# Kernel tuning notes

Measured on AMD Instinct MI355X. Metric: run time of the kernel, lower is better.

The kernel has to match this reference:

```python
import jax, jax.numpy as jnp
import numpy as np

B, ZD, E, L, NL = 64, 512, 512, 8192, 1000


def irm(x, Ws, bs):
    # IRMLinear(d, n_layers=2): stack of residual linear blocks x <- x + Linear(x)
    for W, b in zip(Ws, bs):
        x = x + x @ W.T + b
    return x


def setup_inputs() -> dict:
    key = jax.random.key(0)
    ks = jax.random.split(key, 10)
    s = lambda k, sh: (jax.random.normal(k, sh, jnp.float32) * 0.02)
    return dict(
        z=jax.random.normal(ks[0], (B, ZD), jnp.float32),
        y=jax.random.randint(ks[1], (B,), 0, NL),
        W_yemb=s(ks[2], (E, NL)), b_yemb=jnp.zeros((E,), jnp.float32),
        Wy1=s(ks[3], (E, E)), by1=jnp.zeros((E,), jnp.float32),
        Wy2=s(ks[4], (E, E)), by2=jnp.zeros((E,), jnp.float32),
        Wz1=s(ks[5], (ZD, ZD)), bz1=jnp.zeros((ZD,), jnp.float32),
        Wz2=s(ks[6], (ZD, ZD)), bz2=jnp.zeros((ZD,), jnp.float32),
        W_zlat=s(ks[7], (L, ZD)),          # Linear(z_dim, lat_size, bias=False)
        w_proj=s(ks[8], (E,)),             # Linear(embed_size, 1, bias=False)
    )


def reference(z, y, W_yemb, b_yemb, Wy1, by1, Wy2, by2, Wz1, bz1, Wz2, bz2, W_zlat, w_proj):
    # y: int64 class ids -> one-hot via identity embedding_mat
    yembed = jax.nn.one_hot(y, NL, dtype=jnp.float32)            # [B, NL]
    ye = yembed @ W_yemb.T + b_yemb                               # [B, E]
    ye = irm(ye, [Wy1, Wy2], [by1, by2])                          # [B, E]
    zz = irm(z, [Wz1, Wz2], [bz1, bz2])                           # [B, ZD]
    zl = zz @ W_zlat.T                                            # [B, L]
    # bmm(z[:,:,1], ye[:,1,:]) then lat_proj over embed collapses to a
    # per-batch scalar: lat[b,i] = zl[b,i] * (ye[b] . w_proj)  (same math,
    # avoids the [B, L, E] intermediate)
    s_scal = ye @ w_proj                                          # [B]
    return zl * s_scal[:, None]                                   # [B, L]
```

## Files before the change

### kernel.cpp

```cpp
#include <hip/hip_runtime.h>


#define BB 64
#define DD 512
#define LL 8192
#define NLBL 1000

typedef __attribute__((ext_vector_type(8))) short short8;
typedef __attribute__((ext_vector_type(4))) float f32x4;

__device__ __forceinline__ unsigned short f2bf(float f) {
  unsigned u = __float_as_uint(f);
  return (unsigned short)((u + 0x7fffu + ((u >> 16) & 1u)) >> 16);
}

__device__ __forceinline__ void matvec_block(int eblk, const float* __restrict__ W,
                                             const float* __restrict__ vin,
                                             float* __restrict__ vout) {
  __shared__ float vl[DD];
  __shared__ float red[256];
  int tid = threadIdx.x;
  vl[tid] = vin[tid];
  vl[tid + 256] = vin[tid + 256];
  __syncthreads();
  int el = tid & 31, jg = tid >> 5;
  int e = eblk * 32 + el;
  float acc = 0.f;
  for (int j = jg; j < DD; j += 8)
    acc += W[j * DD + e] * vl[j];
  red[tid] = acc;
  __syncthreads();
  if (tid < 32) {
    float s = vl[eblk * 32 + tid];
#pragma unroll
    for (int g = 0; g < 8; ++g) s += red[g * 32 + tid];
    vout[eblk * 32 + tid] = s;
  }
}

template <int GATHER, int BF16OUT, int JW, int HASBIAS>
__device__ __forceinline__ void gemm_fullk(
    int blk, const float* __restrict__ Ain,
    const float* __restrict__ Wemb, const float* __restrict__ bemb,
    const int* __restrict__ y,
    const float* __restrict__ W, const float* __restrict__ bias,
    float* __restrict__ outf, unsigned short* __restrict__ outh) {
  __shared__ __align__(16) float As[8][DD];
  int tid = threadIdx.x;
  constexpr int NJT = DD / JW;
  int bt = blk / NJT, jt = blk % NJT;
  int b0 = bt * 8, j0 = jt * JW;
  if (GATHER) {
#pragma unroll
    for (int r = 0; r < 8; ++r) {
      int yb = y[b0 + r];
      As[r][tid]       = Wemb[(size_t)tid * NLBL + yb]         + bemb[tid];
      As[r][tid + 256] = Wemb[(size_t)(tid + 256) * NLBL + yb] + bemb[tid + 256];
    }
  } else {
#pragma unroll
    for (int i = 0; i < 4; ++i) {
      int g = tid + i * 256;
      int row = g >> 7, c4 = (g & 127) << 2;
      *(float4*)&As[row][c4] = *(const float4*)&Ain[(size_t)(b0 + row) * DD + c4];
    }
  }
  __syncthreads();
  int jl = tid & 31, bg = tid >> 5;
  constexpr int NO = JW / 32;
  const float* wr[NO];
#pragma unroll
  for (int o = 0; o < NO; ++o) wr[o] = W + (size_t)(j0 + o * 32 + jl) * DD;
  float a0[NO] = {}, a1[NO] = {}, a2[NO] = {}, a3[NO] = {};
#pragma unroll 4
  for (int k4 = 0; k4 < 128; ++k4) {
    float4 av = *(const float4*)&As[bg][k4 << 2];
#pragma unroll
    for (int o = 0; o < NO; ++o) {
      float4 wv = *(const float4*)&wr[o][k4 << 2];
      a0[o] = fmaf(av.x, wv.x, a0[o]);
      a1[o] = fmaf(av.y, wv.y, a1[o]);
      a2[o] = fmaf(av.z, wv.z, a2[o]);
      a3[o] = fmaf(av.w, wv.w, a3[o]);
    }
  }
#pragma unroll
  for (int o = 0; o < NO; ++o) {
    int j = j0 + o * 32 + jl;
    float v = (a0[o] + a1[o]) + (a2[o] + a3[o]) + As[bg][j];
    if (HASBIAS) v += bias[j];
    if (BF16OUT) outh[(size_t)(b0 + bg) * DD + j] = f2bf(v);
    else         outf[(size_t)(b0 + bg) * DD + j] = v;
  }
}

__device__ __forceinline__ void s_block(int cid, const float* __restrict__ GH,
                                        const float* __restrict__ u1,
                                        const float* __restrict__ by1,
                                        const float* __restrict__ by2,
                                        const float* __restrict__ w_proj,
                                        float* __restrict__ sv) {
  __shared__ float red[256];
  __shared__ float d2s;
  int tid = threadIdx.x;
  float p = by1[tid] * u1[tid] + by2[tid] * w_proj[tid] +
            by1[tid + 256] * u1[tid + 256] + by2[tid + 256] * w_proj[tid + 256];
  red[tid] = p;
  __syncthreads();
  if (tid < 64) {
    float s = red[tid] + red[tid + 64] + red[tid + 128] + red[tid + 192];
#pragma unroll
    for (int d = 32; d; d >>= 1) s += __shfl_down(s, d, 64);
    if (tid == 0) d2s = s;
  }
  __syncthreads();
  int bloc = tid >> 6, lane = tid & 63;
  int b = cid * 4 + bloc;
  int e0 = lane * 8;
  float4 g0 = *(const float4*)&GH[(size_t)b * DD + e0];
  float4 g1 = *(const float4*)&GH[(size_t)b * DD + e0 + 4];
  float4 ua = *(const float4*)&u1[e0];
  float4 ub = *(const float4*)&u1[e0 + 4];
  float sg = g0.x * ua.x + g0.y * ua.y + g0.z * ua.z + g0.w * ua.w +
             g1.x * ub.x + g1.y * ub.y + g1.z * ub.z + g1.w * ub.w;
#pragma unroll
  for (int d = 32; d; d >>= 1) sg += __shfl_down(sg, d, 64);
  if (lane == 0) sv[b] = sg + d2s;
}

__global__ __launch_bounds__(256) void k1(
    const float* __restrict__ z, const float* __restrict__ Wz1,
    const float* __restrict__ bz1, float* __restrict__ X1,
    const float* __restrict__ Wy2, const float* __restrict__ w_proj,
    float* __restrict__ u1, const float* __restrict__ W_yemb,
    const float* __restrict__ b_yemb, const int* __restrict__ y,
    const float* __restrict__ Wy1, float* __restrict__ GH) {
  int blk = blockIdx.x;
  if (blk < 64)
    gemm_fullk<1, 0, 64, 0>(blk, nullptr, W_yemb, b_yemb, y, Wy1, nullptr, GH, nullptr);
  else if (blk < 192)
    gemm_fullk<0, 0, 32, 1>(blk - 64, z, nullptr, nullptr, nullptr, Wz1, bz1, X1, nullptr);
  else
    matvec_block(blk - 192, Wy2, w_proj, u1);
}

__global__ __launch_bounds__(256) void k2(
    const float* __restrict__ X1, const float* __restrict__ Wz2,
    const float* __restrict__ bz2, unsigned short* __restrict__ zzs,
    const float* __restrict__ GH, const float* __restrict__ u1,
    const float* __restrict__ by1, const float* __restrict__ by2,
    const float* __restrict__ w_proj, float* __restrict__ sv) {
  int blk = blockIdx.x;
  if (blk < 128)
    gemm_fullk<0, 1, 32, 1>(blk, X1, nullptr, nullptr, nullptr, Wz2, bz2, nullptr, zzs);
  else
    s_block(blk - 128, GH, u1, by1, by2, w_proj, sv);
}

__global__ __launch_bounds__(256) void kC(const unsigned short* __restrict__ zzs,
                                          const float* __restrict__ W,
                                          const float* __restrict__ sv,
                                          float* __restrict__ out) {
  __shared__ __align__(16) unsigned short Bs[16 * 512];
  __shared__ float ss[64];
  int tid = threadIdx.x;
  int l0 = blockIdx.x * 16;
  if (tid < 64) ss[tid] = sv[tid];
#pragma unroll
  for (int i = 0; i < 4; ++i) {
    int gi = tid + i * 256, row = gi >> 6, c = gi & 63;
    const float* src = &W[(size_t)(l0 + row) * DD + c * 8];
    float4 v0 = *(const float4*)src;
    float4 v1 = *(const float4*)(src + 4);
    short8 h = {(short)f2bf(v0.x), (short)f2bf(v0.y), (short)f2bf(v0.z),
                (short)f2bf(v0.w), (short)f2bf(v1.x), (short)f2bf(v1.y),
                (short)f2bf(v1.z), (short)f2bf(v1.w)};
    *(short8*)&Bs[row * DD + ((c ^ (row & 7)) << 3)] = h;
  }
  __syncthreads();
  int wave = tid >> 6, lane = tid & 63, quad = lane >> 4, l15 = lane & 15;
  const unsigned short* arow = zzs + (wave * 16 + l15) * DD + quad * 8;
  f32x4 acc = {};
  short8 apf[4];
#pragma unroll
  for (int p = 0; p < 4; ++p) apf[p] = *(const short8*)(arow + p * 32);
#pragma unroll
  for (int kc = 0; kc < 4; ++kc) {
    short8 cur[4] = {apf[0], apf[1], apf[2], apf[3]};
    if (kc < 3) {
#pragma unroll
      for (int p = 0; p < 4; ++p)
        apf[p] = *(const short8*)(arow + (kc + 1) * 128 + p * 32);
    }
#pragma unroll
    for (int s = 0; s < 4; ++s) {
      int c = kc * 16 + s * 4 + quad;
      short8 bf = *(const short8*)&Bs[l15 * DD + ((c ^ (l15 & 7)) << 3)];
      acc = __builtin_amdgcn_mfma_f32_16x16x32_bf16(cur[s], bf, acc, 0, 0, 0);
    }
  }
#pragma unroll
  for (int reg = 0; reg < 4; ++reg) {
    int b = wave * 16 + quad * 4 + reg;
    out[(size_t)b * LL + l0 + l15] = acc[reg] * ss[b];
  }
}

extern "C" void kernel_launch(void* const* d_in, const int* in_sizes, int n_in,
                              void* d_out, int out_size, void* d_ws, size_t ws_size,
                              hipStream_t stream) {
  const float* z      = (const float*)d_in[0];
  const int*   y      = (const int*)  d_in[1];
  const float* W_yemb = (const float*)d_in[2];
  const float* b_yemb = (const float*)d_in[3];
  const float* Wy1    = (const float*)d_in[4];
  const float* by1    = (const float*)d_in[5];
  const float* Wy2    = (const float*)d_in[6];
  const float* by2    = (const float*)d_in[7];
  const float* Wz1    = (const float*)d_in[8];
  const float* bz1    = (const float*)d_in[9];
  const float* Wz2    = (const float*)d_in[10];
  const float* bz2    = (const float*)d_in[11];
  const float* W_zlat = (const float*)d_in[12];
  const float* w_proj = (const float*)d_in[13];

  float* ws = (float*)d_ws;
  float* X1 = ws;
  float* GH = ws + 32768;
  float* u1 = ws + 65536;
  float* sv = ws + 66048;
  unsigned short* zzs = (unsigned short*)(ws + 66112);
  float* out = (float*)d_out;

  k1<<<208, 256, 0, stream>>>(z, Wz1, bz1, X1, Wy2, w_proj, u1, W_yemb, b_yemb, y, Wy1, GH);
  k2<<<144, 256, 0, stream>>>(X1, Wz2, bz2, zzs, GH, u1, by1, by2, w_proj, sv);
  kC<<<512, 256, 0, stream>>>(zzs, W_zlat, sv, out);
}
```

Before: 146.9 us.

## Stage weight tiles through double-buffered LDS in small GEMM blocks

```diff
diff --git a/kernel.cpp b/kernel.cpp
--- a/kernel.cpp
+++ b/kernel.cpp
@@ -39,17 +39,20 @@
 }
 
 template <int GATHER, int BF16OUT, int JW, int HASBIAS>
-__device__ __forceinline__ void gemm_fullk(
+__device__ __forceinline__ void gemm_fullk2(
     int blk, const float* __restrict__ Ain,
     const float* __restrict__ Wemb, const float* __restrict__ bemb,
     const int* __restrict__ y,
     const float* __restrict__ W, const float* __restrict__ bias,
     float* __restrict__ outf, unsigned short* __restrict__ outh) {
+  constexpr int NO = JW / 32;
+  constexpr int NJT = DD / JW;
   __shared__ __align__(16) float As[8][DD];
-  int tid = threadIdx.x;
-  constexpr int NJT = DD / JW;
+  __shared__ __align__(16) float Ws[2][JW][68];
+  int tid = threadIdx.x;
   int bt = blk / NJT, jt = blk % NJT;
   int b0 = bt * 8, j0 = jt * JW;
+
   if (GATHER) {
 #pragma unroll
     for (int r = 0; r < 8; ++r) {
@@ -65,24 +68,39 @@
       *(float4*)&As[row][c4] = *(const float4*)&Ain[(size_t)(b0 + row) * DD + c4];
     }
   }
-  __syncthreads();
+#pragma unroll
+  for (int i = 0; i < NO * 2; ++i) {
+    int gi = tid + i * 256;
+    int row = gi >> 4, c4 = (gi & 15) << 2;
+    *(float4*)&Ws[0][row][c4] = *(const float4*)&W[(size_t)(j0 + row) * DD + c4];
+  }
+  __syncthreads();
+
   int jl = tid & 31, bg = tid >> 5;
-  constexpr int NO = JW / 32;
-  const float* wr[NO];
-#pragma unroll
-  for (int o = 0; o < NO; ++o) wr[o] = W + (size_t)(j0 + o * 32 + jl) * DD;
   float a0[NO] = {}, a1[NO] = {}, a2[NO] = {}, a3[NO] = {};
-#pragma unroll 4
-  for (int k4 = 0; k4 < 128; ++k4) {
-    float4 av = *(const float4*)&As[bg][k4 << 2];
-#pragma unroll
-    for (int o = 0; o < NO; ++o) {
-      float4 wv = *(const float4*)&wr[o][k4 << 2];
-      a0[o] = fmaf(av.x, wv.x, a0[o]);
-      a1[o] = fmaf(av.y, wv.y, a1[o]);
-      a2[o] = fmaf(av.z, wv.z, a2[o]);
-      a3[o] = fmaf(av.w, wv.w, a3[o]);
-    }
+  for (int c = 0; c < 8; ++c) {
+    if (c < 7) {
+#pragma unroll
+      for (int i = 0; i < NO * 2; ++i) {
+        int gi = tid + i * 256;
+        int row = gi >> 4, c4 = (gi & 15) << 2;
+        *(float4*)&Ws[(c + 1) & 1][row][c4] =
+            *(const float4*)&W[(size_t)(j0 + row) * DD + (c + 1) * 64 + c4];
+      }
+    }
+#pragma unroll
+    for (int k4 = 0; k4 < 16; ++k4) {
+      float4 av = *(const float4*)&As[bg][c * 64 + (k4 << 2)];
+#pragma unroll
+      for (int o = 0; o < NO; ++o) {
+        float4 wv = *(const float4*)&Ws[c & 1][jl + o * 32][k4 << 2];
+        a0[o] = fmaf(av.x, wv.x, a0[o]);
+        a1[o] = fmaf(av.y, wv.y, a1[o]);
+        a2[o] = fmaf(av.z, wv.z, a2[o]);
+        a3[o] = fmaf(av.w, wv.w, a3[o]);
+      }
+    }
+    __syncthreads();
   }
 #pragma unroll
   for (int o = 0; o < NO; ++o) {
@@ -137,9 +155,9 @@
     const float* __restrict__ Wy1, float* __restrict__ GH) {
   int blk = blockIdx.x;
   if (blk < 64)
-    gemm_fullk<1, 0, 64, 0>(blk, nullptr, W_yemb, b_yemb, y, Wy1, nullptr, GH, nullptr);
+    gemm_fullk2<1, 0, 64, 0>(blk, nullptr, W_yemb, b_yemb, y, Wy1, nullptr, GH, nullptr);
   else if (blk < 192)
-    gemm_fullk<0, 0, 32, 1>(blk - 64, z, nullptr, nullptr, nullptr, Wz1, bz1, X1, nullptr);
+    gemm_fullk2<0, 0, 32, 1>(blk - 64, z, nullptr, nullptr, nullptr, Wz1, bz1, X1, nullptr);
   else
     matvec_block(blk - 192, Wy2, w_proj, u1);
 }
@@ -152,7 +170,7 @@
     const float* __restrict__ w_proj, float* __restrict__ sv) {
   int blk = blockIdx.x;
   if (blk < 128)
-    gemm_fullk<0, 1, 32, 1>(blk, X1, nullptr, nullptr, nullptr, Wz2, bz2, nullptr, zzs);
+    gemm_fullk2<0, 1, 32, 1>(blk, X1, nullptr, nullptr, nullptr, Wz2, bz2, nullptr, zzs);
   else
     s_block(blk - 128, GH, u1, by1, by2, w_proj, sv);
 }
```

Measured after the change: 125.4 us. -14.6%, faster.
